# Performance work log

Measured on AMD Instinct MI355X. Metric: run time of the kernel, lower is better.

## Reference

```python
import jax, jax.numpy as jnp
import numpy as np

B, S, D_IN, D_MODEL, H = 4, 2048, 1024, 1024, 16
HD = D_MODEL // H  # head_dim = 64


def setup_inputs() -> dict:
    key = jax.random.key(0)
    ks = jax.random.split(key, 9)
    scale = 1.0 / np.sqrt(D_IN)
    return {
        "Q": jax.random.normal(ks[0], (B, S, D_IN), jnp.float32),
        "V": jax.random.normal(ks[1], (B, S, D_IN), jnp.float32),
        "K": jax.random.normal(ks[2], (B, S, D_IN), jnp.float32),
        "wq": jax.random.uniform(ks[3], (D_IN, D_MODEL), jnp.float32, -scale, scale),
        "bq": jax.random.uniform(ks[4], (D_MODEL,), jnp.float32, -scale, scale),
        "wk": jax.random.uniform(ks[5], (D_IN, D_MODEL), jnp.float32, -scale, scale),
        "bk": jax.random.uniform(ks[6], (D_MODEL,), jnp.float32, -scale, scale),
        "wv": jax.random.uniform(ks[7], (D_IN, D_MODEL), jnp.float32, -scale, scale),
        "bv": jax.random.uniform(ks[8], (D_MODEL,), jnp.float32, -scale, scale),
    }


def _split_heads(x):
    # [B,S,D] -> [B,H,S,HD]
    return x.reshape(B, S, H, HD).transpose(0, 2, 1, 3)


def reference(Q, V, K, wq, bq, wk, bk, wv, bv):
    q = _split_heads(Q @ wq + bq)
    k = _split_heads(K @ wk + bk)
    v = _split_heads(V @ wv + bv)
    scores = jnp.einsum("bhqd,bhkd->bhqk", q, k) / jnp.sqrt(jnp.float32(HD))
    weights = jax.nn.softmax(scores, axis=-1)
    out = jnp.einsum("bhqk,bhkd->bhqd", weights, v)
    return out.transpose(0, 2, 1, 3).reshape(B, S, D_MODEL)
```

## Files before the change

### kernel.cpp

```cpp
#include <hip/hip_runtime.h>
#include <hip/hip_bf16.h>

typedef unsigned short u16;
typedef __attribute__((ext_vector_type(8))) short bf16x8;
typedef __attribute__((ext_vector_type(4))) float f32x4;
typedef __attribute__((ext_vector_type(4))) unsigned short u16x4;
typedef __attribute__((ext_vector_type(2))) unsigned u32x2;

#define NB 4
#define NS 2048
#define DIN 1024
#define DM 1024
#define NH 16
#define HD 64
#define LOG2E 1.44269504f

__device__ __forceinline__ u16 f2bf(float f) {
  union { float f; unsigned u; } x; x.f = f;
  unsigned r = x.u + 0x7fffu + ((x.u >> 16) & 1u);
  return (u16)(r >> 16);
}

__device__ __forceinline__ unsigned pk_bf16(float a, float b) {
  union { __hip_bfloat162 h; unsigned u; } cv;
  cv.h = __float22bfloat162_rn(make_float2(a, b));
  return cv.u;
}

__device__ __forceinline__ void gl_lds16(const u16* g, u16* l) {
  __builtin_amdgcn_global_load_lds((const __attribute__((address_space(1))) void*)g,
                                   (__attribute__((address_space(3))) void*)l, 16, 0, 0);
}

__global__ void cvt_kernel(const float* __restrict__ Qp, const float* __restrict__ Kp,
                           const float* __restrict__ Vp, u16* __restrict__ oq,
                           u16* __restrict__ ok, u16* __restrict__ ov, int n4) {
  const float* s = blockIdx.y == 0 ? Qp : blockIdx.y == 1 ? Kp : Vp;
  u16* d = blockIdx.y == 0 ? oq : blockIdx.y == 1 ? ok : ov;
  int stride = gridDim.x * blockDim.x;
  for (int i = blockIdx.x * blockDim.x + threadIdx.x; i < n4; i += stride) {
    f32x4 v = ((const f32x4*)s)[i];
    u32x2 o;
    o.x = pk_bf16(v.x, v.y);
    o.y = pk_bf16(v.z, v.w);
    ((u32x2*)d)[i] = o;
  }
}

__global__ void wtrans_kernel(const float* __restrict__ wqp, const float* __restrict__ wkp,
                              const float* __restrict__ wvp, u16* __restrict__ oq,
                              u16* __restrict__ ok, u16* __restrict__ ov) {
  const float* W = blockIdx.z == 0 ? wqp : blockIdx.z == 1 ? wkp : wvp;
  u16* Wt = blockIdx.z == 0 ? oq : blockIdx.z == 1 ? ok : ov;
  __shared__ float tile[64][65];
  int n0 = blockIdx.x * 64, k0 = blockIdx.y * 64;
  int t = threadIdx.x;
#pragma unroll
  for (int i = 0; i < 16; i++) {
    int idx = t + i * 256;
    int r = idx >> 6, c = idx & 63;
    tile[r][c] = W[(size_t)(k0 + r) * DM + n0 + c];
  }
  __syncthreads();
#pragma unroll
  for (int i = 0; i < 16; i++) {
    int idx = t + i * 256;
    int r = idx >> 6, c = idx & 63;
    Wt[(size_t)(n0 + r) * DIN + k0 + c] = f2bf(tile[c][r]);
  }
}

__global__ __launch_bounds__(256) void proj_kernel(
    const u16* __restrict__ Xq, const u16* __restrict__ Xk, const u16* __restrict__ Xv,
    const u16* __restrict__ Wtq, const u16* __restrict__ Wtk, const u16* __restrict__ Wtv,
    const float* __restrict__ bq, const float* __restrict__ bk, const float* __restrict__ bv,
    u16* __restrict__ oq, u16* __restrict__ ok, u16* __restrict__ ov) {
  __shared__ __align__(16) u16 Abuf[128 * 64];
  __shared__ __align__(16) u16 Bbuf[128 * 64];
  const int bid = blockIdx.x;
  const int xr = bid & 7;
  const int nt = (bid >> 3) & 7;
  const int mt = (bid >> 6) & 7;
  const int z  = bid >> 9;
  const int m0 = (mt * 8 + xr) * 128, n0 = nt * 128;
  const u16* X  = z == 0 ? Xq : z == 1 ? Xk : Xv;
  const u16* Wt = z == 0 ? Wtq : z == 1 ? Wtk : Wtv;
  const float* bias = z == 0 ? bq : z == 1 ? bk : bv;
  u16* out = z == 0 ? oq : z == 1 ? ok : ov;
  const int t = threadIdx.x, lane = t & 63, w = t >> 6;
  const int c = lane & 15, g = lane >> 4;
  const int wm = (w >> 1) * 64, wn = (w & 1) * 64;
  f32x4 acc[4][4] = {};
  for (int k0 = 0; k0 < DIN; k0 += 64) {
#pragma unroll
    for (int i = 0; i < 4; i++) {
      int idx = (w * 4 + i) * 64 + lane;
      int row = idx >> 3;
      int srck = (idx & 7) ^ (row & 7);
      gl_lds16(&X [(size_t)(m0 + row) * DIN + k0 + srck * 8], &Abuf[(w * 4 + i) * 512]);
      gl_lds16(&Wt[(size_t)(n0 + row) * DIN + k0 + srck * 8], &Bbuf[(w * 4 + i) * 512]);
    }
    __syncthreads();
#pragma unroll
    for (int ks = 0; ks < 2; ks++) {
      bf16x8 xf[4], wf[4];
      int chn = ((ks * 4 + g) ^ (c & 7)) * 8;
#pragma unroll
      for (int a = 0; a < 4; a++) {
        xf[a] = *(const bf16x8*)&Abuf[(wm + a * 16 + c) * 64 + chn];
        wf[a] = *(const bf16x8*)&Bbuf[(wn + a * 16 + c) * 64 + chn];
      }
      if (z < 2) {
#pragma unroll
        for (int i = 0; i < 4; i++)
#pragma unroll
          for (int j = 0; j < 4; j++)
            acc[i][j] = __builtin_amdgcn_mfma_f32_16x16x32_bf16(wf[i], xf[j], acc[i][j], 0, 0, 0);
      } else {
#pragma unroll
        for (int i = 0; i < 4; i++)
#pragma unroll
          for (int j = 0; j < 4; j++)
            acc[i][j] = __builtin_amdgcn_mfma_f32_16x16x32_bf16(xf[i], wf[j], acc[i][j], 0, 0, 0);
      }
    }
    __syncthreads();
  }
  if (z < 2) {
    const float sc = (z == 0) ? 0.125f * LOG2E : 1.0f;
#pragma unroll
    for (int i = 0; i < 4; i++) {
      int nb = n0 + wn + i * 16 + g * 4;
      int h = nb >> 6, d0 = nb & 63;
      f32x4 bv4 = *(const f32x4*)&bias[nb];
#pragma unroll
      for (int j = 0; j < 4; j++) {
        int mm = m0 + wm + j * 16 + c;
        int b = mm >> 11, s = mm & 2047;
        u16x4 pk;
#pragma unroll
        for (int r = 0; r < 4; r++) pk[r] = f2bf((acc[i][j][r] + bv4[r]) * sc);
        *(u16x4*)&out[((size_t)(b * NH + h) * NS + s) * HD + d0] = pk;
      }
    }
  } else {
#pragma unroll
    for (int j = 0; j < 4; j++) {
      int n = n0 + wn + j * 16 + c;
      int h = n >> 6, d = n & 63;
      float bvs = bias[n];
#pragma unroll
      for (int i = 0; i < 4; i++) {
        int mb = m0 + wm + i * 16 + g * 4;
        int b = mb >> 11, s0 = mb & 2047;
        u16x4 pk;
#pragma unroll
        for (int r = 0; r < 4; r++) pk[r] = f2bf(acc[i][j][r] + bvs);
        *(u16x4*)&out[((size_t)(b * NH + h) * HD + d) * NS + s0] = pk;
      }
    }
  }
}

#define NG 2
__global__ __launch_bounds__(256, 2) void attn_kernel(
    const u16* __restrict__ q, const u16* __restrict__ k, const u16* __restrict__ vT,
    float* __restrict__ out) {
  __shared__ __align__(16) u16 kt[64 * 64];
  __shared__ __align__(16) u16 vt[64 * 64];
  __shared__ __align__(16) u16 pt_all[4][NG * 16 * 64];
  const int bid = blockIdx.x;
  const int xr = bid & 7;
  const int qc = (bid >> 3) & 15;
  const int h8 = bid >> 7;
  const int bh = xr + 8 * h8;
  const int t = threadIdx.x, lane = t & 63, w = t >> 6;
  const int c = lane & 15, g = lane >> 4;
  const int q0 = qc * 128 + w * 32;
  u16* pt = pt_all[w];
  const u16* qsrc = q + ((size_t)bh * NS + q0) * HD;
  const u16* ksrc = k + (size_t)bh * NS * HD;
  const u16* vsrc = vT + (size_t)bh * HD * NS;
  const int srow = lane >> 3;
  const int skc = (lane & 7) ^ srow;
  bf16x8 qf[NG][2];
#pragma unroll
  for (int grp = 0; grp < NG; grp++)
#pragma unroll
    for (int ks = 0; ks < 2; ks++)
      qf[grp][ks] = *(const bf16x8*)&qsrc[(grp * 16 + c) * HD + ks * 32 + g * 8];
  bf16x8 ones;
#pragma unroll
  for (int i = 0; i < 8; i++) ones[i] = (short)0x3F80;
  f32x4 o[NG][4] = {};
  f32x4 ol[NG] = {};
  for (int kt0 = 0; kt0 < NS; kt0 += 64) {
#pragma unroll
    for (int j = 0; j < 2; j++) {
      int row = w * 16 + j * 8 + srow;
      gl_lds16(&ksrc[(size_t)(kt0 + row) * HD + skc * 8], &kt[(w * 16 + j * 8) * 64]);
      gl_lds16(&vsrc[(size_t)row * NS + kt0 + skc * 8], &vt[(w * 16 + j * 8) * 64]);
    }
    __syncthreads();
    bf16x8 kf[4][2], vf[4][2];
#pragma unroll
    for (int kg = 0; kg < 4; kg++)
#pragma unroll
      for (int ks = 0; ks < 2; ks++) {
        kf[kg][ks] = *(const bf16x8*)&kt[(kg * 16 + c) * 64 + (((ks * 4 + g) ^ (c & 7)) * 8)];
        vf[kg][ks] = *(const bf16x8*)&vt[(kg * 16 + c) * 64 + (((ks * 4 + g) ^ (c & 7)) * 8)];
      }
#pragma unroll
    for (int grp = 0; grp < NG; grp++) {
      f32x4 s4[4] = {};
      __builtin_amdgcn_s_setprio(1);
#pragma unroll
      for (int ks = 0; ks < 2; ks++)
#pragma unroll
        for (int kg = 0; kg < 4; kg++)
          s4[kg] = __builtin_amdgcn_mfma_f32_16x16x32_bf16(kf[kg][ks], qf[grp][ks], s4[kg], 0, 0, 0);
      __builtin_amdgcn_s_setprio(0);
#pragma unroll
      for (int kg = 0; kg < 4; kg++) {
        u32x2 pk;
        pk.x = pk_bf16(__builtin_amdgcn_exp2f(s4[kg][0]), __builtin_amdgcn_exp2f(s4[kg][1]));
        pk.y = pk_bf16(__builtin_amdgcn_exp2f(s4[kg][2]), __builtin_amdgcn_exp2f(s4[kg][3]));
        *(u32x2*)&pt[(grp * 16 + c) * 64 + (((kg * 2 + (g >> 1)) ^ (c & 7)) * 8) + (g & 1) * 4] = pk;
      }
    }
#pragma unroll
    for (int grp = 0; grp < NG; grp++) {
      bf16x8 pf[2];
#pragma unroll
      for (int ks = 0; ks < 2; ks++)
        pf[ks] = *(const bf16x8*)&pt[(grp * 16 + c) * 64 + (((ks * 4 + g) ^ (c & 7)) * 8)];
      __builtin_amdgcn_s_setprio(1);
#pragma unroll
      for (int ks = 0; ks < 2; ks++) {
#pragma unroll
        for (int dj = 0; dj < 4; dj++)
          o[grp][dj] = __builtin_amdgcn_mfma_f32_16x16x32_bf16(vf[dj][ks], pf[ks], o[grp][dj], 0, 0, 0);
        ol[grp] = __builtin_amdgcn_mfma_f32_16x16x32_bf16(ones, pf[ks], ol[grp], 0, 0, 0);
      }
      __builtin_amdgcn_s_setprio(0);
    }
    __syncthreads();
  }
  const int b = bh >> 4, h = bh & 15;
#pragma unroll
  for (int grp = 0; grp < NG; grp++) {
    float inv = 1.f / ol[grp][0];
    int s = q0 + grp * 16 + c;
#pragma unroll
    for (int dj = 0; dj < 4; dj++) {
      f32x4 ov = o[grp][dj] * inv;
      *(f32x4*)&out[((size_t)b * NS + s) * DM + h * HD + dj * 16 + g * 4] = ov;
    }
  }
}

extern "C" void kernel_launch(void* const* d_in, const int* in_sizes, int n_in,
                              void* d_out, int out_size, void* d_ws, size_t ws_size,
                              hipStream_t stream) {
  const float* Q  = (const float*)d_in[0];
  const float* V  = (const float*)d_in[1];
  const float* K  = (const float*)d_in[2];
  const float* wq = (const float*)d_in[3];
  const float* bq = (const float*)d_in[4];
  const float* wk = (const float*)d_in[5];
  const float* bk = (const float*)d_in[6];
  const float* wv = (const float*)d_in[7];
  const float* bv = (const float*)d_in[8];
  float* out = (float*)d_out;
  char* ws = (char*)d_ws;
  const size_t NX = (size_t)NB * NS * DIN;
  const size_t XB = NX * 2;
  const size_t WB = (size_t)DIN * DM * 2;
  u16* Xq   = (u16*)(ws);
  u16* Xk   = (u16*)(ws + XB);
  u16* Xv   = (u16*)(ws + 2 * XB);
  u16* Wtq  = (u16*)(ws + 3 * XB);
  u16* Wtk  = (u16*)(ws + 3 * XB + WB);
  u16* Wtv  = (u16*)(ws + 3 * XB + 2 * WB);
  u16* qws  = (u16*)(ws + 3 * XB + 3 * WB);
  u16* kws  = (u16*)(ws + 4 * XB + 3 * WB);
  u16* vTws = (u16*)(ws + 5 * XB + 3 * WB);
  const int n4 = (int)(NX / 4);
  cvt_kernel<<<dim3(1024, 3), 256, 0, stream>>>(Q, K, V, Xq, Xk, Xv, n4);
  wtrans_kernel<<<dim3(16, 16, 3), 256, 0, stream>>>(wq, wk, wv, Wtq, Wtk, Wtv);
  proj_kernel<<<1536, 256, 0, stream>>>(Xq, Xk, Xv, Wtq, Wtk, Wtv,
                                        bq, bk, bv, qws, kws, vTws);
  attn_kernel<<<1024, 256, 0, stream>>>(qws, kws, vTws, out);
}
```

Before: 311.0 us.

## Double-buffer K/V tiles in attention kernel with async prefetch

Adds a second LDS buffer for K and V tiles so the next tile's global-to-LDS load is issued before computing on the current tile. The wait uses explicit vmcnt counts and raw barriers in place of __syncthreads. V fragment loads are also moved to just before the PV MFMAs, one ks slice at a time, to lower register pressure. This is meant to hide global memory latency. In exchange it doubles K/V LDS use, which may affect occupancy at two blocks per CU, and it relies on the hand-set vmcnt value matching the number of outstanding loads.

New measurement: 320.4 us. +3.0%, slower.

```diff
diff --git a/kernel.cpp b/kernel.cpp
--- a/kernel.cpp
+++ b/kernel.cpp
@@ -166,8 +166,8 @@
 __global__ __launch_bounds__(256, 2) void attn_kernel(
     const u16* __restrict__ q, const u16* __restrict__ k, const u16* __restrict__ vT,
     float* __restrict__ out) {
-  __shared__ __align__(16) u16 kt[64 * 64];
-  __shared__ __align__(16) u16 vt[64 * 64];
+  __shared__ __align__(16) u16 kt[2][64 * 64];
+  __shared__ __align__(16) u16 vt[2][64 * 64];
   __shared__ __align__(16) u16 pt_all[4][NG * 16 * 64];
   const int bid = blockIdx.x;
   const int xr = bid & 7;
@@ -194,22 +194,37 @@
   for (int i = 0; i < 8; i++) ones[i] = (short)0x3F80;
   f32x4 o[NG][4] = {};
   f32x4 ol[NG] = {};
+
+#define STAGE(buf, kk0)                                                              \
+  {                                                                                  \
+    _Pragma("unroll") for (int j = 0; j < 2; j++) {                                  \
+      int row = w * 16 + j * 8 + srow;                                               \
+      gl_lds16(&ksrc[(size_t)((kk0) + row) * HD + skc * 8],                          \
+               &kt[buf][(w * 16 + j * 8) * 64]);                                     \
+      gl_lds16(&vsrc[(size_t)row * NS + (kk0) + skc * 8],                            \
+               &vt[buf][(w * 16 + j * 8) * 64]);                                     \
+    }                                                                                \
+  }
+
+  STAGE(0, 0);
+  int cur = 0;
   for (int kt0 = 0; kt0 < NS; kt0 += 64) {
-#pragma unroll
-    for (int j = 0; j < 2; j++) {
-      int row = w * 16 + j * 8 + srow;
-      gl_lds16(&ksrc[(size_t)(kt0 + row) * HD + skc * 8], &kt[(w * 16 + j * 8) * 64]);
-      gl_lds16(&vsrc[(size_t)row * NS + kt0 + skc * 8], &vt[(w * 16 + j * 8) * 64]);
-    }
-    __syncthreads();
-    bf16x8 kf[4][2], vf[4][2];
+    if (kt0 + 64 < NS) {
+      STAGE(cur ^ 1, kt0 + 64);
+      asm volatile("s_waitcnt vmcnt(4)" ::: "memory");
+    } else {
+      asm volatile("s_waitcnt vmcnt(0)" ::: "memory");
+    }
+    __builtin_amdgcn_s_barrier();
+    __builtin_amdgcn_sched_barrier(0);
+    const u16* ktc = kt[cur];
+    const u16* vtc = vt[cur];
+    bf16x8 kf[4][2];
 #pragma unroll
     for (int kg = 0; kg < 4; kg++)
 #pragma unroll
-      for (int ks = 0; ks < 2; ks++) {
-        kf[kg][ks] = *(const bf16x8*)&kt[(kg * 16 + c) * 64 + (((ks * 4 + g) ^ (c & 7)) * 8)];
-        vf[kg][ks] = *(const bf16x8*)&vt[(kg * 16 + c) * 64 + (((ks * 4 + g) ^ (c & 7)) * 8)];
-      }
+      for (int ks = 0; ks < 2; ks++)
+        kf[kg][ks] = *(const bf16x8*)&ktc[(kg * 16 + c) * 64 + (((ks * 4 + g) ^ (c & 7)) * 8)];
 #pragma unroll
     for (int grp = 0; grp < NG; grp++) {
       f32x4 s4[4] = {};
@@ -229,23 +244,28 @@
       }
     }
 #pragma unroll
-    for (int grp = 0; grp < NG; grp++) {
-      bf16x8 pf[2];
-#pragma unroll
-      for (int ks = 0; ks < 2; ks++)
-        pf[ks] = *(const bf16x8*)&pt[(grp * 16 + c) * 64 + (((ks * 4 + g) ^ (c & 7)) * 8)];
-      __builtin_amdgcn_s_setprio(1);
-#pragma unroll
-      for (int ks = 0; ks < 2; ks++) {
+    for (int ks = 0; ks < 2; ks++) {
+      bf16x8 vf4[4];
+#pragma unroll
+      for (int dj = 0; dj < 4; dj++)
+        vf4[dj] = *(const bf16x8*)&vtc[(dj * 16 + c) * 64 + (((ks * 4 + g) ^ (c & 7)) * 8)];
+#pragma unroll
+      for (int grp = 0; grp < NG; grp++) {
+        bf16x8 pf = *(const bf16x8*)&pt[(grp * 16 + c) * 64 + (((ks * 4 + g) ^ (c & 7)) * 8)];
+        __builtin_amdgcn_s_setprio(1);
 #pragma unroll
         for (int dj = 0; dj < 4; dj++)
-          o[grp][dj] = __builtin_amdgcn_mfma_f32_16x16x32_bf16(vf[dj][ks], pf[ks], o[grp][dj], 0, 0, 0);
-        ol[grp] = __builtin_amdgcn_mfma_f32_16x16x32_bf16(ones, pf[ks], ol[grp], 0, 0, 0);
-      }
-      __builtin_amdgcn_s_setprio(0);
-    }
-    __syncthreads();
-  }
+          o[grp][dj] = __builtin_amdgcn_mfma_f32_16x16x32_bf16(vf4[dj], pf, o[grp][dj], 0, 0, 0);
+        ol[grp] = __builtin_amdgcn_mfma_f32_16x16x32_bf16(ones, pf, ol[grp], 0, 0, 0);
+        __builtin_amdgcn_s_setprio(0);
+      }
+    }
+    asm volatile("s_waitcnt lgkmcnt(0)" ::: "memory");
+    __builtin_amdgcn_s_barrier();
+    __builtin_amdgcn_sched_barrier(0);
+    cur ^= 1;
+  }
+#undef STAGE
   const int b = bh >> 4, h = bh & 15;
 #pragma unroll
   for (int grp = 0; grp < NG; grp++) {
```

## Load K/V fragments straight from global memory and merge prep kernels

Applied to the files above, without the earlier changes.

The attention kernel no longer stages K and V tiles in LDS through global_load_lds with block-wide barriers. Each wave now reads its MFMA fragments directly from global memory and relies on L1/L2 for reuse, which removes both __syncthreads per key tile and frees LDS. The PV loop is reordered to run ks-major. Separately, the input conversion and the weight transpose are merged into one launch to save a kernel launch. The risks are that every wave issues redundant global loads of the same K/V data, and that load latency becomes exposed without explicit staging.

Measured after the change: 446.0 us. +43.4%, slower.

```diff
diff --git a/kernel.cpp b/kernel.cpp
--- a/kernel.cpp
+++ b/kernel.cpp
@@ -32,41 +32,45 @@
                                    (__attribute__((address_space(3))) void*)l, 16, 0, 0);
 }
 
-__global__ void cvt_kernel(const float* __restrict__ Qp, const float* __restrict__ Kp,
-                           const float* __restrict__ Vp, u16* __restrict__ oq,
-                           u16* __restrict__ ok, u16* __restrict__ ov, int n4) {
-  const float* s = blockIdx.y == 0 ? Qp : blockIdx.y == 1 ? Kp : Vp;
-  u16* d = blockIdx.y == 0 ? oq : blockIdx.y == 1 ? ok : ov;
-  int stride = gridDim.x * blockDim.x;
-  for (int i = blockIdx.x * blockDim.x + threadIdx.x; i < n4; i += stride) {
-    f32x4 v = ((const f32x4*)s)[i];
-    u32x2 o;
-    o.x = pk_bf16(v.x, v.y);
-    o.y = pk_bf16(v.z, v.w);
-    ((u32x2*)d)[i] = o;
-  }
-}
-
-__global__ void wtrans_kernel(const float* __restrict__ wqp, const float* __restrict__ wkp,
-                              const float* __restrict__ wvp, u16* __restrict__ oq,
-                              u16* __restrict__ ok, u16* __restrict__ ov) {
-  const float* W = blockIdx.z == 0 ? wqp : blockIdx.z == 1 ? wkp : wvp;
-  u16* Wt = blockIdx.z == 0 ? oq : blockIdx.z == 1 ? ok : ov;
+__global__ void prep_kernel(const float* __restrict__ Qp, const float* __restrict__ Kp,
+                            const float* __restrict__ Vp, u16* __restrict__ oq,
+                            u16* __restrict__ ok, u16* __restrict__ ov,
+                            const float* __restrict__ wqp, const float* __restrict__ wkp,
+                            const float* __restrict__ wvp, u16* __restrict__ owq,
+                            u16* __restrict__ owk, u16* __restrict__ owv, int n4) {
   __shared__ float tile[64][65];
-  int n0 = blockIdx.x * 64, k0 = blockIdx.y * 64;
-  int t = threadIdx.x;
-#pragma unroll
-  for (int i = 0; i < 16; i++) {
-    int idx = t + i * 256;
-    int r = idx >> 6, c = idx & 63;
-    tile[r][c] = W[(size_t)(k0 + r) * DM + n0 + c];
-  }
-  __syncthreads();
-#pragma unroll
-  for (int i = 0; i < 16; i++) {
-    int idx = t + i * 256;
-    int r = idx >> 6, c = idx & 63;
-    Wt[(size_t)(n0 + r) * DIN + k0 + c] = f2bf(tile[c][r]);
+  const int b = blockIdx.x, t = threadIdx.x;
+  if (b < 3072) {
+    const int ten = b >> 10, bx = b & 1023;
+    const float* s = ten == 0 ? Qp : ten == 1 ? Kp : Vp;
+    u16* d = ten == 0 ? oq : ten == 1 ? ok : ov;
+    int stride = 1024 * 256;
+    for (int i = bx * 256 + t; i < n4; i += stride) {
+      f32x4 v = ((const f32x4*)s)[i];
+      u32x2 o;
+      o.x = pk_bf16(v.x, v.y);
+      o.y = pk_bf16(v.z, v.w);
+      ((u32x2*)d)[i] = o;
+    }
+  } else {
+    const int wt = b - 3072;
+    const int z = wt >> 8, rem = wt & 255;
+    const float* W = z == 0 ? wqp : z == 1 ? wkp : wvp;
+    u16* Wt = z == 0 ? owq : z == 1 ? owk : owv;
+    int n0 = (rem & 15) * 64, k0 = (rem >> 4) * 64;
+#pragma unroll
+    for (int i = 0; i < 16; i++) {
+      int idx = t + i * 256;
+      int r = idx >> 6, c = idx & 63;
+      tile[r][c] = W[(size_t)(k0 + r) * DM + n0 + c];
+    }
+    __syncthreads();
+#pragma unroll
+    for (int i = 0; i < 16; i++) {
+      int idx = t + i * 256;
+      int r = idx >> 6, c = idx & 63;
+      Wt[(size_t)(n0 + r) * DIN + k0 + c] = f2bf(tile[c][r]);
+    }
   }
 }
 
@@ -166,8 +170,6 @@
 __global__ __launch_bounds__(256, 2) void attn_kernel(
     const u16* __restrict__ q, const u16* __restrict__ k, const u16* __restrict__ vT,
     float* __restrict__ out) {
-  __shared__ __align__(16) u16 kt[64 * 64];
-  __shared__ __align__(16) u16 vt[64 * 64];
   __shared__ __align__(16) u16 pt_all[4][NG * 16 * 64];
   const int bid = blockIdx.x;
   const int xr = bid & 7;
@@ -181,8 +183,6 @@
   const u16* qsrc = q + ((size_t)bh * NS + q0) * HD;
   const u16* ksrc = k + (size_t)bh * NS * HD;
   const u16* vsrc = vT + (size_t)bh * HD * NS;
-  const int srow = lane >> 3;
-  const int skc = (lane & 7) ^ srow;
   bf16x8 qf[NG][2];
 #pragma unroll
   for (int grp = 0; grp < NG; grp++)
@@ -194,22 +194,16 @@
   for (int i = 0; i < 8; i++) ones[i] = (short)0x3F80;
   f32x4 o[NG][4] = {};
   f32x4 ol[NG] = {};
+#pragma unroll 1
   for (int kt0 = 0; kt0 < NS; kt0 += 64) {
-#pragma unroll
-    for (int j = 0; j < 2; j++) {
-      int row = w * 16 + j * 8 + srow;
-      gl_lds16(&ksrc[(size_t)(kt0 + row) * HD + skc * 8], &kt[(w * 16 + j * 8) * 64]);
-      gl_lds16(&vsrc[(size_t)row * NS + kt0 + skc * 8], &vt[(w * 16 + j * 8) * 64]);
-    }
-    __syncthreads();
-    bf16x8 kf[4][2], vf[4][2];
+    const u16* kp = ksrc + (size_t)kt0 * HD;
+    const u16* vp = vsrc + kt0;
+    bf16x8 kf[4][2];
 #pragma unroll
     for (int kg = 0; kg < 4; kg++)
 #pragma unroll
-      for (int ks = 0; ks < 2; ks++) {
-        kf[kg][ks] = *(const bf16x8*)&kt[(kg * 16 + c) * 64 + (((ks * 4 + g) ^ (c & 7)) * 8)];
-        vf[kg][ks] = *(const bf16x8*)&vt[(kg * 16 + c) * 64 + (((ks * 4 + g) ^ (c & 7)) * 8)];
-      }
+      for (int ks = 0; ks < 2; ks++)
+        kf[kg][ks] = *(const bf16x8*)&kp[(size_t)(kg * 16 + c) * HD + ks * 32 + g * 8];
 #pragma unroll
     for (int grp = 0; grp < NG; grp++) {
       f32x4 s4[4] = {};
@@ -228,23 +222,25 @@
         *(u32x2*)&pt[(grp * 16 + c) * 64 + (((kg * 2 + (g >> 1)) ^ (c & 7)) * 8) + (g & 1) * 4] = pk;
       }
     }
-#pragma unroll
-    for (int grp = 0; grp < NG; grp++) {
-      bf16x8 pf[2];
+    bf16x8 vf[4][2];
+#pragma unroll
+    for (int dj = 0; dj < 4; dj++)
 #pragma unroll
       for (int ks = 0; ks < 2; ks++)
-        pf[ks] = *(const bf16x8*)&pt[(grp * 16 + c) * 64 + (((ks * 4 + g) ^ (c & 7)) * 8)];
-      __builtin_amdgcn_s_setprio(1);
-#pragma unroll
-      for (int ks = 0; ks < 2; ks++) {
+        vf[dj][ks] = *(const bf16x8*)&vp[(size_t)(dj * 16 + c) * NS + ks * 32 + g * 8];
+#pragma unroll
+    for (int ks = 0; ks < 2; ks++) {
+#pragma unroll
+      for (int grp = 0; grp < NG; grp++) {
+        bf16x8 pf = *(const bf16x8*)&pt[(grp * 16 + c) * 64 + (((ks * 4 + g) ^ (c & 7)) * 8)];
+        __builtin_amdgcn_s_setprio(1);
 #pragma unroll
         for (int dj = 0; dj < 4; dj++)
-          o[grp][dj] = __builtin_amdgcn_mfma_f32_16x16x32_bf16(vf[dj][ks], pf[ks], o[grp][dj], 0, 0, 0);
-        ol[grp] = __builtin_amdgcn_mfma_f32_16x16x32_bf16(ones, pf[ks], ol[grp], 0, 0, 0);
-      }
-      __builtin_amdgcn_s_setprio(0);
-    }
-    __syncthreads();
+          o[grp][dj] = __builtin_amdgcn_mfma_f32_16x16x32_bf16(vf[dj][ks], pf, o[grp][dj], 0, 0, 0);
+        ol[grp] = __builtin_amdgcn_mfma_f32_16x16x32_bf16(ones, pf, ol[grp], 0, 0, 0);
+        __builtin_amdgcn_s_setprio(0);
+      }
+    }
   }
   const int b = bh >> 4, h = bh & 15;
 #pragma unroll
@@ -286,8 +282,8 @@
   u16* kws  = (u16*)(ws + 4 * XB + 3 * WB);
   u16* vTws = (u16*)(ws + 5 * XB + 3 * WB);
   const int n4 = (int)(NX / 4);
-  cvt_kernel<<<dim3(1024, 3), 256, 0, stream>>>(Q, K, V, Xq, Xk, Xv, n4);
-  wtrans_kernel<<<dim3(16, 16, 3), 256, 0, stream>>>(wq, wk, wv, Wtq, Wtk, Wtv);
+  prep_kernel<<<3840, 256, 0, stream>>>(Q, K, V, Xq, Xk, Xv,
+                                        wq, wk, wv, Wtq, Wtk, Wtv, n4);
   proj_kernel<<<1536, 256, 0, stream>>>(Xq, Xk, Xv, Wtq, Wtk, Wtv,
                                         bq, bk, bv, qws, kws, vTws);
   attn_kernel<<<1024, 256, 0, stream>>>(qws, kws, vTws, out);
```
